# Kernel optimization log

Measured on AMD Instinct MI355X. Metric: run time of the kernel, lower is better.

Reference implementation:

```python
import jax, jax.numpy as jnp
import numpy as np

N = 10000
E = 640000
C = 128   # in_channels
H = 512   # hidden_dim
O = 128   # out_channels


def setup_inputs() -> dict:
    key = jax.random.key(0)
    k1, k2, k3, k4, k5, k6, k7 = jax.random.split(key, 7)
    x = jax.random.normal(k1, (N, C), dtype=jnp.float32)
    edge_index = jax.random.randint(k2, (2, E), 0, N, dtype=jnp.int64)
    # MLP params (Linear(2C, H) -> ReLU -> Linear(H, O)), torch default init scale
    w1 = jax.random.uniform(k3, (2 * C, H), jnp.float32, -1, 1) / np.sqrt(2 * C)
    b1 = jax.random.uniform(k4, (H,), jnp.float32, -1, 1) / np.sqrt(2 * C)
    w2 = jax.random.uniform(k5, (H, O), jnp.float32, -1, 1) / np.sqrt(H)
    b2 = jax.random.uniform(k6, (O,), jnp.float32, -1, 1) / np.sqrt(H)
    return {"x": x, "edge_index": edge_index, "w1": w1, "b1": b1, "w2": w2, "b2": b2}


def reference(x, edge_index, w1, b1, w2, b2):
    row, col = edge_index[0], edge_index[1]
    # scatter_mean: mean of source features x[col] into destination row
    summed = jax.ops.segment_sum(x[col], row, num_segments=N)          # [N, C]
    count = jax.ops.segment_sum(jnp.ones((E,), x.dtype), row, num_segments=N)
    neighbor_mean = summed / jnp.maximum(count, 1.0)[:, None]          # [N, C]
    h = jnp.concatenate([x, neighbor_mean], axis=1)                    # [N, 2C]
    h = jax.nn.relu(h @ w1 + b1)                                       # [N, H]
    return h @ w2 + b2                                                 # [N, O]
```

## Files before the change

### kernel.cpp

```cpp
#include <hip/hip_runtime.h>

#define C_IN 128
#define H_DIM 512
#define O_DIM 128
#define CAP   192
#define PAD   16
#define BM    32

typedef __attribute__((ext_vector_type(8))) short short8;
typedef __attribute__((ext_vector_type(4))) float f32x4;

__device__ inline unsigned short f2bf(float f) {
    unsigned int u = __float_as_uint(f);
    unsigned int r = (u + 0x7FFF + ((u >> 16) & 1)) >> 16;
    return (unsigned short)r;
}
__device__ inline float bf2f(unsigned short s) {
    return __uint_as_float(((unsigned int)s) << 16);
}

__device__ inline void tr_tile(const float* __restrict__ src, unsigned short* __restrict__ dst,
                               int R, int Ccols, int bx, int by) {
    __shared__ float tile[32][33];
    const int c0 = bx * 32, r0 = by * 32;
    const int tx = threadIdx.x & 31, ty = threadIdx.x >> 5;
#pragma unroll
    for (int i = 0; i < 32; i += 8)
        tile[ty + i][tx] = src[(long)(r0 + ty + i) * Ccols + c0 + tx];
    __syncthreads();
#pragma unroll
    for (int i = 0; i < 32; i += 8)
        dst[(long)(c0 + ty + i) * R + r0 + tx] = f2bf(tile[tx][ty + i]);
}

__global__ __launch_bounds__(256)
void prep_kernel(const float* __restrict__ w1, unsigned short* __restrict__ w1t,
                 const float* __restrict__ w2, unsigned short* __restrict__ w2t,
                 const float* __restrict__ x, unsigned short* __restrict__ h0,
                 int* __restrict__ cnt_p, int N) {
    if (blockIdx.z == 0) {
        if (blockIdx.y < (2 * C_IN) / 32) tr_tile(w1, w1t, 2 * C_IN, H_DIM, blockIdx.x, blockIdx.y);
    } else if (blockIdx.z == 1) {
        if (blockIdx.x < O_DIM / 32) tr_tile(w2, w2t, H_DIM, O_DIM, blockIdx.x, blockIdx.y);
    } else {
        const int bid = blockIdx.y * 16 + blockIdx.x;
        const int gtid = bid * 256 + threadIdx.x;
        const int nf4 = N * C_IN / 4;
        for (int i = gtid; i < nf4; i += 65536) {
            int n = i >> 5, c4 = i & 31;
            float4 v = ((const float4*)x)[i];
            ushort4 s;
            s.x = f2bf(v.x); s.y = f2bf(v.y); s.z = f2bf(v.z); s.w = f2bf(v.w);
            *(ushort4*)(h0 + (long)n * (2 * C_IN) + c4 * 4) = s;
        }
        const int n4 = N * PAD / 4;
        for (int i = gtid; i < n4; i += 65536)
            ((int4*)cnt_p)[i] = make_int4(0, 0, 0, 0);
    }
}

__global__ void fill_kernel(const int* __restrict__ ei, int* __restrict__ cnt_p,
                            unsigned short* __restrict__ bucket, int E) {
    int e = blockIdx.x * blockDim.x + threadIdx.x;
    if (e >= E) return;
    int row = ei[e];
    int col = ei[E + e];
    int slot = atomicAdd(&cnt_p[row * PAD], 1);
    if (slot < CAP) bucket[(long)row * CAP + slot] = (unsigned short)col;
}

__global__ __launch_bounds__(256)
void gather_kernel(const unsigned short* __restrict__ bucket,
                   const int* __restrict__ cnt_p, unsigned short* __restrict__ h0,
                   int N) {
    const int lane = threadIdx.x & 63;
    const int n = blockIdx.x * 4 + (threadIdx.x >> 6);
    if (n >= N) return;
    const int half = lane >> 5;
    const int l32 = lane & 31;
    const int degt = cnt_p[n * PAD];
    const int deg = min(degt, CAP);
    const long base = (long)n * CAP;

    float a0 = 0.f, a1 = 0.f, a2 = 0.f, a3 = 0.f;
    int e = 0;
    for (; e + 4 <= deg; e += 4) {
        int c0 = bucket[base + e + half];
        int c1 = bucket[base + e + 2 + half];
        ushort4 u0 = *(const ushort4*)(h0 + (long)c0 * (2 * C_IN) + l32 * 4);
        ushort4 u1 = *(const ushort4*)(h0 + (long)c1 * (2 * C_IN) + l32 * 4);
        a0 += bf2f(u0.x) + bf2f(u1.x);
        a1 += bf2f(u0.y) + bf2f(u1.y);
        a2 += bf2f(u0.z) + bf2f(u1.z);
        a3 += bf2f(u0.w) + bf2f(u1.w);
    }
    for (; e + 2 <= deg; e += 2) {
        int c = bucket[base + e + half];
        ushort4 u = *(const ushort4*)(h0 + (long)c * (2 * C_IN) + l32 * 4);
        a0 += bf2f(u.x); a1 += bf2f(u.y); a2 += bf2f(u.z); a3 += bf2f(u.w);
    }
    if (e < deg && half == 0) {
        int c = bucket[base + e];
        ushort4 u = *(const ushort4*)(h0 + (long)c * (2 * C_IN) + l32 * 4);
        a0 += bf2f(u.x); a1 += bf2f(u.y); a2 += bf2f(u.z); a3 += bf2f(u.w);
    }
    a0 += __shfl_xor(a0, 32, 64);
    a1 += __shfl_xor(a1, 32, 64);
    a2 += __shfl_xor(a2, 32, 64);
    a3 += __shfl_xor(a3, 32, 64);

    if (half == 0) {
        float inv = 1.0f / fmaxf((float)degt, 1.0f);
        ushort4 mv;
        mv.x = f2bf(a0 * inv);
        mv.y = f2bf(a1 * inv);
        mv.z = f2bf(a2 * inv);
        mv.w = f2bf(a3 * inv);
        *(ushort4*)(h0 + (long)n * (2 * C_IN) + C_IN + l32 * 4) = mv;
    }
}

__global__ __launch_bounds__(256)
void fused_mlp(const unsigned short* __restrict__ h0,
               const unsigned short* __restrict__ w1t,
               const float* __restrict__ b1,
               const unsigned short* __restrict__ w2t,
               const float* __restrict__ b2,
               float* __restrict__ out, int M) {
    __shared__ __align__(16) unsigned short Bs[32][264];
    __shared__ __align__(16) unsigned short h1s[32][520];

    const int t = threadIdx.x;
    const int m0 = blockIdx.x * BM;
    const int lane = t & 63;
    const int w = t >> 6;
    const int l16 = lane & 15;
    const int q = lane >> 4;
    const int q8 = q * 8;

    const int mf1 = w >> 1;
    const int nf1 = w & 1;

    short8 a_reg[8];
    {
        int gm = m0 + mf1 * 16 + l16;
        if (gm < M) {
            const unsigned short* ap = h0 + (long)gm * (2 * C_IN) + q8;
#pragma unroll
            for (int s = 0; s < 8; s++) a_reg[s] = *(const short8*)(ap + s * 32);
        } else {
#pragma unroll
            for (int s = 0; s < 8; s++) a_reg[s] = short8{};
        }
    }

    for (int nc = 0; nc < 16; nc++) {
        {
            const unsigned short* src = w1t + (long)nc * 32 * 256;
#pragma unroll
            for (int i = 0; i < 4; i++) {
                int cid = t + i * 256;
                int r = cid >> 5, c8 = (cid & 31) * 8;
                *(short8*)&Bs[r][c8] = *(const short8*)(src + r * 256 + c8);
            }
        }
        __syncthreads();
        f32x4 acc = {};
#pragma unroll
        for (int s = 0; s < 8; s++) {
            short8 b = *(const short8*)&Bs[nf1 * 16 + l16][s * 32 + q8];
            acc = __builtin_amdgcn_mfma_f32_16x16x32_bf16(a_reg[s], b, acc, 0, 0, 0);
        }
        {
            int coll = nf1 * 16 + l16;
            float bb = b1[nc * 32 + coll];
#pragma unroll
            for (int r = 0; r < 4; r++) {
                int m = mf1 * 16 + q * 4 + r;
                float v = fmaxf(acc[r] + bb, 0.f);
                h1s[m][nc * 32 + coll] = f2bf(v);
            }
        }
        __syncthreads();
    }

    f32x4 acc2[2][2] = {};
    const int wn = w * 32;
#pragma unroll
    for (int ks = 0; ks < 16; ks++) {
        short8 a0 = *(const short8*)&h1s[l16][ks * 32 + q8];
        short8 a1 = *(const short8*)&h1s[16 + l16][ks * 32 + q8];
        short8 b0 = *(const short8*)(w2t + (long)(wn + l16) * H_DIM + ks * 32 + q8);
        short8 b1v = *(const short8*)(w2t + (long)(wn + 16 + l16) * H_DIM + ks * 32 + q8);
        acc2[0][0] = __builtin_amdgcn_mfma_f32_16x16x32_bf16(a0, b0, acc2[0][0], 0, 0, 0);
        acc2[0][1] = __builtin_amdgcn_mfma_f32_16x16x32_bf16(a0, b1v, acc2[0][1], 0, 0, 0);
        acc2[1][0] = __builtin_amdgcn_mfma_f32_16x16x32_bf16(a1, b0, acc2[1][0], 0, 0, 0);
        acc2[1][1] = __builtin_amdgcn_mfma_f32_16x16x32_bf16(a1, b1v, acc2[1][1], 0, 0, 0);
    }
#pragma unroll
    for (int mf = 0; mf < 2; mf++) {
#pragma unroll
        for (int nf = 0; nf < 2; nf++) {
            int gn = wn + nf * 16 + l16;
            float bb = b2[gn];
#pragma unroll
            for (int r = 0; r < 4; r++) {
                int gm = m0 + mf * 16 + q * 4 + r;
                if (gm < M) out[(long)gm * O_DIM + gn] = acc2[mf][nf][r] + bb;
            }
        }
    }
}

extern "C" void kernel_launch(void* const* d_in, const int* in_sizes, int n_in,
                              void* d_out, int out_size, void* d_ws, size_t ws_size,
                              hipStream_t stream) {
    const float* x  = (const float*)d_in[0];
    const int*   ei = (const int*)d_in[1];
    const float* w1 = (const float*)d_in[2];
    const float* b1 = (const float*)d_in[3];
    const float* w2 = (const float*)d_in[4];
    const float* b2 = (const float*)d_in[5];
    float* out = (float*)d_out;

    const int N = in_sizes[0] / C_IN;
    const int E = in_sizes[1] / 2;

    unsigned short* h0b = (unsigned short*)d_ws;
    unsigned short* w1t = h0b + (size_t)N * (2 * C_IN);
    unsigned short* w2t = w1t + (size_t)H_DIM * (2 * C_IN);
    int* cnt_p = (int*)(w2t + (size_t)O_DIM * H_DIM);
    unsigned short* bucket = (unsigned short*)(cnt_p + (size_t)N * PAD);

    prep_kernel<<<dim3(16, 16, 3), 256, 0, stream>>>(w1, w1t, w2, w2t, x, h0b, cnt_p, N);
    fill_kernel<<<(E + 255) / 256, 256, 0, stream>>>(ei, cnt_p, bucket, E);
    gather_kernel<<<(N + 3) / 4, 256, 0, stream>>>(bucket, cnt_p, h0b, N);
    fused_mlp<<<(N + BM - 1) / BM, 256, 0, stream>>>(h0b, w1t, b1, w2t, b2, out, N);
}
```

Before: 146.8 us.

## Widen gather loads to 16 bytes and restructure MLP tile to 16 rows

The gather kernel now has each lane load eight bf16 values (16 bytes) and processes four neighbours per step across lane quarters, reducing with two shuffles. The fused MLP switches to 16-row tiles. Each wave computes a 128-column slice of the hidden layer reading W1 directly from global memory, which removes the per-chunk shared staging and the 32 barriers. In exchange the MLP launches twice as many blocks and loads W1/W2 from global (L2) more often per row processed.

```diff
diff --git a/kernel.cpp b/kernel.cpp
--- a/kernel.cpp
+++ b/kernel.cpp
@@ -5,7 +5,7 @@
 #define O_DIM 128
 #define CAP   192
 #define PAD   16
-#define BM    32
+#define BM    16
 
 typedef __attribute__((ext_vector_type(8))) short short8;
 typedef __attribute__((ext_vector_type(4))) float f32x4;
@@ -76,59 +76,61 @@
     const int lane = threadIdx.x & 63;
     const int n = blockIdx.x * 4 + (threadIdx.x >> 6);
     if (n >= N) return;
-    const int half = lane >> 5;
-    const int l32 = lane & 31;
+    const int g = lane >> 4;
+    const int l16 = lane & 15;
     const int degt = cnt_p[n * PAD];
     const int deg = min(degt, CAP);
     const long base = (long)n * CAP;
 
-    float a0 = 0.f, a1 = 0.f, a2 = 0.f, a3 = 0.f;
+    float acc[8] = {};
     int e = 0;
-    for (; e + 4 <= deg; e += 4) {
-        int c0 = bucket[base + e + half];
-        int c1 = bucket[base + e + 2 + half];
-        ushort4 u0 = *(const ushort4*)(h0 + (long)c0 * (2 * C_IN) + l32 * 4);
-        ushort4 u1 = *(const ushort4*)(h0 + (long)c1 * (2 * C_IN) + l32 * 4);
-        a0 += bf2f(u0.x) + bf2f(u1.x);
-        a1 += bf2f(u0.y) + bf2f(u1.y);
-        a2 += bf2f(u0.z) + bf2f(u1.z);
-        a3 += bf2f(u0.w) + bf2f(u1.w);
-    }
-    for (; e + 2 <= deg; e += 2) {
-        int c = bucket[base + e + half];
-        ushort4 u = *(const ushort4*)(h0 + (long)c * (2 * C_IN) + l32 * 4);
-        a0 += bf2f(u.x); a1 += bf2f(u.y); a2 += bf2f(u.z); a3 += bf2f(u.w);
-    }
-    if (e < deg && half == 0) {
-        int c = bucket[base + e];
-        ushort4 u = *(const ushort4*)(h0 + (long)c * (2 * C_IN) + l32 * 4);
-        a0 += bf2f(u.x); a1 += bf2f(u.y); a2 += bf2f(u.z); a3 += bf2f(u.w);
-    }
-    a0 += __shfl_xor(a0, 32, 64);
-    a1 += __shfl_xor(a1, 32, 64);
-    a2 += __shfl_xor(a2, 32, 64);
-    a3 += __shfl_xor(a3, 32, 64);
-
-    if (half == 0) {
+    for (; e + 8 <= deg; e += 8) {
+        int c0 = bucket[base + e + g];
+        int c1 = bucket[base + e + 4 + g];
+        short8 u0 = *(const short8*)(h0 + (long)c0 * (2 * C_IN) + l16 * 8);
+        short8 u1 = *(const short8*)(h0 + (long)c1 * (2 * C_IN) + l16 * 8);
+#pragma unroll
+        for (int j = 0; j < 8; j++)
+            acc[j] += bf2f((unsigned short)u0[j]) + bf2f((unsigned short)u1[j]);
+    }
+    if (e + 4 <= deg) {
+        int c = bucket[base + e + g];
+        short8 u = *(const short8*)(h0 + (long)c * (2 * C_IN) + l16 * 8);
+#pragma unroll
+        for (int j = 0; j < 8; j++) acc[j] += bf2f((unsigned short)u[j]);
+        e += 4;
+    }
+    {
+        int rem = deg - e;
+        if (g < rem) {
+            int c = bucket[base + e + g];
+            short8 u = *(const short8*)(h0 + (long)c * (2 * C_IN) + l16 * 8);
+#pragma unroll
+            for (int j = 0; j < 8; j++) acc[j] += bf2f((unsigned short)u[j]);
+        }
+    }
+#pragma unroll
+    for (int j = 0; j < 8; j++) {
+        acc[j] += __shfl_xor(acc[j], 16, 64);
+        acc[j] += __shfl_xor(acc[j], 32, 64);
+    }
+    if (lane < 16) {
         float inv = 1.0f / fmaxf((float)degt, 1.0f);
-        ushort4 mv;
-        mv.x = f2bf(a0 * inv);
-        mv.y = f2bf(a1 * inv);
-        mv.z = f2bf(a2 * inv);
-        mv.w = f2bf(a3 * inv);
-        *(ushort4*)(h0 + (long)n * (2 * C_IN) + C_IN + l32 * 4) = mv;
+        short8 mv;
+#pragma unroll
+        for (int j = 0; j < 8; j++) mv[j] = (short)f2bf(acc[j] * inv);
+        *(short8*)(h0 + (long)n * (2 * C_IN) + C_IN + l16 * 8) = mv;
     }
 }
 
 __global__ __launch_bounds__(256)
 void fused_mlp(const unsigned short* __restrict__ h0,
                const unsigned short* __restrict__ w1t,
-               const float* __restrict__ b1,
+               const float* __restrict__ bias1,
                const unsigned short* __restrict__ w2t,
-               const float* __restrict__ b2,
+               const float* __restrict__ bias2,
                float* __restrict__ out, int M) {
-    __shared__ __align__(16) unsigned short Bs[32][264];
-    __shared__ __align__(16) unsigned short h1s[32][520];
+    __shared__ __align__(16) unsigned short h1s[BM][520];
 
     const int t = threadIdx.x;
     const int m0 = blockIdx.x * BM;
@@ -138,12 +140,9 @@
     const int q = lane >> 4;
     const int q8 = q * 8;
 
-    const int mf1 = w >> 1;
-    const int nf1 = w & 1;
-
     short8 a_reg[8];
     {
-        int gm = m0 + mf1 * 16 + l16;
+        int gm = m0 + l16;
         if (gm < M) {
             const unsigned short* ap = h0 + (long)gm * (2 * C_IN) + q8;
 #pragma unroll
@@ -154,60 +153,46 @@
         }
     }
 
-    for (int nc = 0; nc < 16; nc++) {
-        {
-            const unsigned short* src = w1t + (long)nc * 32 * 256;
-#pragma unroll
-            for (int i = 0; i < 4; i++) {
-                int cid = t + i * 256;
-                int r = cid >> 5, c8 = (cid & 31) * 8;
-                *(short8*)&Bs[r][c8] = *(const short8*)(src + r * 256 + c8);
-            }
-        }
-        __syncthreads();
-        f32x4 acc = {};
+#pragma unroll
+    for (int nc = 0; nc < 4; nc++) {
+        const int colbase = w * 128 + nc * 32;
+        f32x4 acc0 = {}, acc1 = {};
 #pragma unroll
         for (int s = 0; s < 8; s++) {
-            short8 b = *(const short8*)&Bs[nf1 * 16 + l16][s * 32 + q8];
-            acc = __builtin_amdgcn_mfma_f32_16x16x32_bf16(a_reg[s], b, acc, 0, 0, 0);
-        }
-        {
-            int coll = nf1 * 16 + l16;
-            float bb = b1[nc * 32 + coll];
-#pragma unroll
-            for (int r = 0; r < 4; r++) {
-                int m = mf1 * 16 + q * 4 + r;
-                float v = fmaxf(acc[r] + bb, 0.f);
-                h1s[m][nc * 32 + coll] = f2bf(v);
-            }
-        }
-        __syncthreads();
-    }
-
-    f32x4 acc2[2][2] = {};
+            short8 b0 = *(const short8*)(w1t + (long)(colbase + l16) * 256 + s * 32 + q8);
+            short8 b1 = *(const short8*)(w1t + (long)(colbase + 16 + l16) * 256 + s * 32 + q8);
+            acc0 = __builtin_amdgcn_mfma_f32_16x16x32_bf16(a_reg[s], b0, acc0, 0, 0, 0);
+            acc1 = __builtin_amdgcn_mfma_f32_16x16x32_bf16(a_reg[s], b1, acc1, 0, 0, 0);
+        }
+        float bb0 = bias1[colbase + l16];
+        float bb1 = bias1[colbase + 16 + l16];
+#pragma unroll
+        for (int r = 0; r < 4; r++) {
+            int m = q * 4 + r;
+            h1s[m][colbase + l16]      = f2bf(fmaxf(acc0[r] + bb0, 0.f));
+            h1s[m][colbase + 16 + l16] = f2bf(fmaxf(acc1[r] + bb1, 0.f));
+        }
+    }
+    __syncthreads();
+
+    f32x4 acc2[2] = {};
     const int wn = w * 32;
 #pragma unroll
     for (int ks = 0; ks < 16; ks++) {
-        short8 a0 = *(const short8*)&h1s[l16][ks * 32 + q8];
-        short8 a1 = *(const short8*)&h1s[16 + l16][ks * 32 + q8];
+        short8 a  = *(const short8*)&h1s[l16][ks * 32 + q8];
         short8 b0 = *(const short8*)(w2t + (long)(wn + l16) * H_DIM + ks * 32 + q8);
-        short8 b1v = *(const short8*)(w2t + (long)(wn + 16 + l16) * H_DIM + ks * 32 + q8);
-        acc2[0][0] = __builtin_amdgcn_mfma_f32_16x16x32_bf16(a0, b0, acc2[0][0], 0, 0, 0);
-        acc2[0][1] = __builtin_amdgcn_mfma_f32_16x16x32_bf16(a0, b1v, acc2[0][1], 0, 0, 0);
-        acc2[1][0] = __builtin_amdgcn_mfma_f32_16x16x32_bf16(a1, b0, acc2[1][0], 0, 0, 0);
-        acc2[1][1] = __builtin_amdgcn_mfma_f32_16x16x32_bf16(a1, b1v, acc2[1][1], 0, 0, 0);
-    }
-#pragma unroll
-    for (int mf = 0; mf < 2; mf++) {
-#pragma unroll
-        for (int nf = 0; nf < 2; nf++) {
-            int gn = wn + nf * 16 + l16;
-            float bb = b2[gn];
-#pragma unroll
-            for (int r = 0; r < 4; r++) {
-                int gm = m0 + mf * 16 + q * 4 + r;
-                if (gm < M) out[(long)gm * O_DIM + gn] = acc2[mf][nf][r] + bb;
-            }
+        short8 b1 = *(const short8*)(w2t + (long)(wn + 16 + l16) * H_DIM + ks * 32 + q8);
+        acc2[0] = __builtin_amdgcn_mfma_f32_16x16x32_bf16(a, b0, acc2[0], 0, 0, 0);
+        acc2[1] = __builtin_amdgcn_mfma_f32_16x16x32_bf16(a, b1, acc2[1], 0, 0, 0);
+    }
+#pragma unroll
+    for (int nf = 0; nf < 2; nf++) {
+        int gn = wn + nf * 16 + l16;
+        float bb = bias2[gn];
+#pragma unroll
+        for (int r = 0; r < 4; r++) {
+            int gm = m0 + q * 4 + r;
+            if (gm < M) out[(long)gm * O_DIM + gn] = acc2[nf][r] + bb;
         }
     }
 }
```

Result: slower. 151.1 us (+2.9%).
